# Kernel tuning notes

Hardware: AMD Instinct MI355X
Metric: run time of the kernel (lower is better)

The kernel has to match this reference:

```python
import jax, jax.numpy as jnp
import numpy as np

N_NODES = 50000
N_EDGES = 600000
D = 128
N_GRAPHS = 500


def setup_inputs() -> dict:
    key = jax.random.key(0)
    ks = jax.random.split(key, 8)
    node_feats = jax.random.normal(ks[0], (N_NODES, D), dtype=jnp.float32)
    W1 = jax.random.normal(ks[1], (D, D), dtype=jnp.float32) * (1.0 / np.sqrt(D))
    b1 = jnp.zeros((D,), dtype=jnp.float32)
    W2 = jax.random.normal(ks[2], (D, D), dtype=jnp.float32) * (1.0 / np.sqrt(D))
    b2 = jnp.zeros((D,), dtype=jnp.float32)
    src = jax.random.randint(ks[3], (N_EDGES,), 0, N_NODES, dtype=jnp.int32)
    dst = jax.random.randint(ks[4], (N_EDGES,), 0, N_NODES, dtype=jnp.int32)
    graph_ids = jnp.sort(jax.random.randint(ks[5], (N_NODES,), 0, N_GRAPHS, dtype=jnp.int32))
    return {"node_feats": node_feats, "W1": W1, "b1": b1, "W2": W2, "b2": b2,
            "src": src, "dst": dst, "graph_ids": graph_ids}


def _graph_conv(h, W, b, src, dst, norm_src, norm_dst, n_nodes):
    # DGL GraphConv, norm='both': D_in^{-1/2} A D_out^{-1/2} X W + b
    hs = h * norm_src[:, None]                     # (N, D) scale by out-degree^-1/2
    m = jax.ops.segment_sum(hs[src], dst, num_segments=n_nodes)  # sparse aggregate
    return (m * norm_dst[:, None]) @ W + b


def reference(node_feats, W1, b1, W2, b2, src, dst, graph_ids):
    n = node_feats.shape[0]
    ones_e = jnp.ones(src.shape, dtype=node_feats.dtype)
    deg_out = jnp.maximum(jax.ops.segment_sum(ones_e, src, num_segments=n), 1.0)
    deg_in = jnp.maximum(jax.ops.segment_sum(ones_e, dst, num_segments=n), 1.0)
    norm_src = deg_out ** -0.5
    norm_dst = deg_in ** -0.5
    # NOTE: original code builds num_layers-1 = 2 GraphConv layers for num_layers=3
    h = jax.nn.relu(_graph_conv(node_feats, W1, b1, src, dst, norm_src, norm_dst, n))
    h = jax.nn.relu(_graph_conv(h, W2, b2, src, dst, norm_src, norm_dst, n))
    # AvgPooling: per-graph mean of node features
    sums = jax.ops.segment_sum(h, graph_ids, num_segments=N_GRAPHS)
    counts = jnp.maximum(
        jax.ops.segment_sum(jnp.ones((n,), h.dtype), graph_ids, num_segments=N_GRAPHS), 1.0)
    return sums / counts[:, None]
```

## Files before the change

kernel.cpp:

```cpp
#include <hip/hip_runtime.h>

#define D 128

typedef __attribute__((ext_vector_type(8))) short bf16x8;
typedef __attribute__((ext_vector_type(4))) float f32x4;

__device__ __forceinline__ unsigned int f32_to_bf16_rne(float x) {
    unsigned int u = __float_as_uint(x);
    return (u + 0x7FFFu + ((u >> 16) & 1u)) >> 16;
}
__device__ __forceinline__ float bf16_val(float x) {
    return __uint_as_float(f32_to_bf16_rne(x) << 16);
}

__global__ void scatter_count_wprep_kernel(
    const int* __restrict__ src, const int* __restrict__ dst,
    int* __restrict__ cnt_out, int* __restrict__ deg_in,
    unsigned short* __restrict__ bucket, int E, int S, int eblocks,
    const float* __restrict__ W1, const float* __restrict__ W2,
    unsigned short* __restrict__ wt) {
    if ((int)blockIdx.x < eblocks) {
        int e = blockIdx.x * 256 + threadIdx.x;
        if (e < E) {
            int s = src[e];
            int d = dst[e];
            int pos = atomicAdd(&deg_in[d], 1);
            if (pos < S) bucket[(size_t)d * S + pos] = (unsigned short)s;
            atomicAdd(&cnt_out[s], 1);
        }
    } else {
        int i = (blockIdx.x - eblocks) * 256 + threadIdx.x;
        if (i < 2 * 16384) {
            int w = i >> 14, idx = i & 16383;
            int k = idx >> 7, col = idx & 127;
            float v = (w == 0 ? W1 : W2)[idx];
            unsigned int hi = f32_to_bf16_rne(v);
            float lo = v - __uint_as_float(hi << 16);
            int kc = k >> 5, quad = (k >> 3) & 3, j = k & 7;
            size_t slot = (size_t)kc * 4096 + quad * 1024 + col * 8 + j;
            wt[(size_t)w * 32768 + slot] = (unsigned short)hi;
            wt[(size_t)w * 32768 + 16384 + slot] = (unsigned short)f32_to_bf16_rne(lo);
        }
    }
}

__global__ void prep_kernel(const int* __restrict__ cnt_out, const int* __restrict__ cnt_in,
                            float* __restrict__ norm_src, float* __restrict__ norm_dst,
                            const float2* __restrict__ x, unsigned int* __restrict__ xb,
                            int N, int n2, int nbA) {
    int b = blockIdx.x;
    if (b < nbA) {
        int i = b * 256 + threadIdx.x;
        if (i < N) {
            norm_src[i] = 1.0f / sqrtf(fmaxf((float)cnt_out[i], 1.0f));
            norm_dst[i] = 1.0f / sqrtf(fmaxf((float)cnt_in[i], 1.0f));
        }
    } else {
        int i = (b - nbA) * 256 + threadIdx.x;
        if (i < n2) {
            int row = i >> 6;
            float s = 1.0f / sqrtf(fmaxf((float)cnt_out[row], 1.0f));
            float2 v = x[i];
            xb[i] = f32_to_bf16_rne(v.x * s) | (f32_to_bf16_rne(v.y * s) << 16);
        }
    }
}

#define AGG_STEP(J) do {                                                       \
        int sj = ss[J];                                                        \
        uint2 uj = featb2[(size_t)sj * 32 + c];                                \
        acc.x += __uint_as_float(uj.x << 16);                                  \
        acc.y += __uint_as_float(uj.x & 0xFFFF0000u);                          \
        acc.z += __uint_as_float(uj.y << 16);                                  \
        acc.w += __uint_as_float(uj.y & 0xFFFF0000u);                          \
    } while (0)

template <bool OUT_BF16>
__global__ __launch_bounds__(512, 8) void agg_mfma_kernel(
    const uint2* __restrict__ featb2, const float* __restrict__ norm_src,
    const float* __restrict__ norm_dst, const int* __restrict__ deg_in,
    const unsigned short* __restrict__ bucket,
    const unsigned short* __restrict__ wthi, const unsigned short* __restrict__ wtlo,
    const float* __restrict__ bias, void* __restrict__ outp, int N, int S) {
    __shared__ unsigned int mtp[2][16][68];
    int node0 = blockIdx.x * 16;
    int ng = threadIdx.x >> 5;
    int c  = threadIdx.x & 31;
    int node = node0 + ng;

    float4 acc = make_float4(0.f, 0.f, 0.f, 0.f);
    if (node < N) {
        int len = min(deg_in[node], S);
        const unsigned short* row = bucket + (size_t)node * S;
        int e = 0;
        for (; e + 8 <= len; e += 8) {
            ushort4 sa = *(const ushort4*)(row + e);
            ushort4 sb = *(const ushort4*)(row + e + 4);
            int ss[8] = {sa.x, sa.y, sa.z, sa.w, sb.x, sb.y, sb.z, sb.w};
            AGG_STEP(0); AGG_STEP(1); AGG_STEP(2); AGG_STEP(3);
            AGG_STEP(4); AGG_STEP(5); AGG_STEP(6); AGG_STEP(7);
        }
        for (; e + 4 <= len; e += 4) {
            ushort4 sa = *(const ushort4*)(row + e);
            int ss[4] = {sa.x, sa.y, sa.z, sa.w};
            AGG_STEP(0); AGG_STEP(1); AGG_STEP(2); AGG_STEP(3);
        }
        for (; e < len; e++) {
            int ss[1] = {row[e]};
            AGG_STEP(0);
        }
    }
    float hx = bf16_val(acc.x), hy = bf16_val(acc.y);
    float hz = bf16_val(acc.z), hw = bf16_val(acc.w);
    mtp[0][ng][2 * c]     = f32_to_bf16_rne(acc.x) | (f32_to_bf16_rne(acc.y) << 16);
    mtp[0][ng][2 * c + 1] = f32_to_bf16_rne(acc.z) | (f32_to_bf16_rne(acc.w) << 16);
    mtp[1][ng][2 * c]     = f32_to_bf16_rne(acc.x - hx) | (f32_to_bf16_rne(acc.y - hy) << 16);
    mtp[1][ng][2 * c + 1] = f32_to_bf16_rne(acc.z - hz) | (f32_to_bf16_rne(acc.w - hw) << 16);
    __syncthreads();

    int lane = threadIdx.x & 63;
    int wv   = threadIdx.x >> 6;
    int n16  = lane & 15;
    int quad = lane >> 4;
    int col  = wv * 16 + n16;
    f32x4 dacc = {0.f, 0.f, 0.f, 0.f};
#pragma unroll
    for (int kc = 0; kc < 4; kc++) {
        int ko = kc * 32 + quad * 8;
        int bo = kc * 4096 + quad * 1024 + col * 8;
        bf16x8 ahi = *(const bf16x8*)((const unsigned short*)mtp[0][n16] + ko);
        bf16x8 alo = *(const bf16x8*)((const unsigned short*)mtp[1][n16] + ko);
        bf16x8 bhi = *(const bf16x8*)(wthi + bo);
        bf16x8 blo = *(const bf16x8*)(wtlo + bo);
        dacc = __builtin_amdgcn_mfma_f32_16x16x32_bf16(ahi, bhi, dacc, 0, 0, 0);
        dacc = __builtin_amdgcn_mfma_f32_16x16x32_bf16(ahi, blo, dacc, 0, 0, 0);
        dacc = __builtin_amdgcn_mfma_f32_16x16x32_bf16(alo, bhi, dacc, 0, 0, 0);
    }
    float bv = bias[col];
#pragma unroll
    for (int r = 0; r < 4; r++) {
        int n = node0 + quad * 4 + r;
        if (n < N) {
            float v = fmaxf(fmaf(dacc[r], norm_dst[n], bv), 0.f);
            if (OUT_BF16) {
                ((unsigned short*)outp)[(size_t)n * D + col] =
                    (unsigned short)f32_to_bf16_rne(v * norm_src[n]);
            } else {
                ((float*)outp)[(size_t)n * D + col] = v;
            }
        }
    }
}

__global__ void pool_kernel(const float* __restrict__ h, const int* __restrict__ gids,
                            float* __restrict__ out, int N, int G) {
    __shared__ float part[128];
    int g = blockIdx.x;
    int f = threadIdx.x & 127;
    int half = threadIdx.x >> 7;
    int lo = 0, hi = N;
    while (lo < hi) { int mid = (lo + hi) >> 1; if (gids[mid] < g) lo = mid + 1; else hi = mid; }
    int start = lo;
    hi = N;
    while (lo < hi) { int mid = (lo + hi) >> 1; if (gids[mid] < g + 1) lo = mid + 1; else hi = mid; }
    int end = lo;

    float s0 = 0.f, s1 = 0.f, s2 = 0.f, s3 = 0.f;
    int n = start + half;
    for (; n + 6 < end; n += 8) {
        s0 += h[(size_t)(n + 0) * D + f];
        s1 += h[(size_t)(n + 2) * D + f];
        s2 += h[(size_t)(n + 4) * D + f];
        s3 += h[(size_t)(n + 6) * D + f];
    }
    for (; n < end; n += 2) s0 += h[(size_t)n * D + f];
    float s = (s0 + s1) + (s2 + s3);
    if (half == 1) part[f] = s;
    __syncthreads();
    if (half == 0) {
        float cnt = (float)(end - start);
        out[(size_t)g * D + f] = (s + part[f]) / fmaxf(cnt, 1.0f);
    }
}

extern "C" void kernel_launch(void* const* d_in, const int* in_sizes, int n_in,
                              void* d_out, int out_size, void* d_ws, size_t ws_size,
                              hipStream_t stream) {
    const float* node_feats = (const float*)d_in[0];
    const float* W1 = (const float*)d_in[1];
    const float* b1 = (const float*)d_in[2];
    const float* W2 = (const float*)d_in[3];
    const float* b2 = (const float*)d_in[4];
    const int*   src = (const int*)d_in[5];
    const int*   dst = (const int*)d_in[6];
    const int*   gid = (const int*)d_in[7];

    int N = in_sizes[7];
    int E = in_sizes[5];
    int G = out_size / D;

    size_t npad = ((size_t)N + 255) & ~(size_t)255;

    int S = 64;
    while (S > 32) {
        size_t need = (4 * npad + npad * (size_t)(S / 2)
                       + (size_t)N * D / 2 * 2
                       + (size_t)N * D
                       + 32768) * sizeof(float);
        if (need <= ws_size) break;
        S -= 16;
    }

    float* ws       = (float*)d_ws;
    float* norm_src = ws;
    float* norm_dst = ws + npad;
    int*   cnt_out  = (int*)(ws + 2 * npad);
    int*   deg_in   = (int*)(ws + 3 * npad);
    unsigned short* bucket = (unsigned short*)(ws + 4 * npad);
    unsigned int* xb  = (unsigned int*)(ws + 4 * npad + npad * (size_t)(S / 2));
    unsigned int* h1b = xb + (size_t)N * D / 2;
    float* h2       = (float*)(h1b + (size_t)N * D / 2);
    unsigned short* wt = (unsigned short*)(h2 + (size_t)N * D);
    float* out      = (float*)d_out;

    (void)hipMemsetAsync(cnt_out, 0, 2 * npad * sizeof(int), stream);
    int eblocks = (E + 255) / 256;
    int wblocks = (2 * 16384 + 255) / 256;
    scatter_count_wprep_kernel<<<eblocks + wblocks, 256, 0, stream>>>(
        src, dst, cnt_out, deg_in, bucket, E, S, eblocks, W1, W2, wt);
    int n2 = N * (D / 2);
    int nbA = (N + 255) / 256;
    int nbB = (n2 + 255) / 256;
    prep_kernel<<<nbA + nbB, 256, 0, stream>>>(cnt_out, deg_in, norm_src, norm_dst,
                                               (const float2*)node_feats, xb, N, n2, nbA);

    int blocks = (N + 15) / 16;

    agg_mfma_kernel<true><<<blocks, 512, 0, stream>>>(
        (const uint2*)xb, norm_src, norm_dst, deg_in, bucket,
        wt, wt + 16384, b1, h1b, N, S);
    agg_mfma_kernel<false><<<blocks, 512, 0, stream>>>(
        (const uint2*)h1b, norm_src, norm_dst, deg_in, bucket,
        wt + 32768, wt + 49152, b2, h2, N, S);

    pool_kernel<<<G, 256, 0, stream>>>(h2, gid, out, N, G);
}
```

Baseline: 223.2 us.

## Partition degree counting and bucketing per XCC to avoid cross-die atomics

The edge scatter now reads the hardware XCC id and does its degree and out-count atomics on per-XCC partitioned arrays, using workgroup-scope relaxed atomics, with per-XCC 16-slot buckets. A new merge kernel sums the eight partitions and compacts the per-XCC buckets into the final adjacency bucket. The aim is to keep atomics in each die's local L2 instead of paying for coherent device-wide atomics. In exchange it adds a kernel launch, a larger memset, and extra memory traffic. Workgroup-scope atomics are only correct if all blocks on an XCC share the same L2, and any XCC partition with more than 16 in-edges for a node now drops edges.

```diff
diff --git a/kernel.cpp b/kernel.cpp
--- a/kernel.cpp
+++ b/kernel.cpp
@@ -1,6 +1,7 @@
 #include <hip/hip_runtime.h>
 
 #define D 128
+#define S8 16
 
 typedef __attribute__((ext_vector_type(8))) short bf16x8;
 typedef __attribute__((ext_vector_type(4))) float f32x4;
@@ -15,18 +16,26 @@
 
 __global__ void scatter_count_wprep_kernel(
     const int* __restrict__ src, const int* __restrict__ dst,
-    int* __restrict__ cnt_out, int* __restrict__ deg_in,
-    unsigned short* __restrict__ bucket, int E, int S, int eblocks,
+    int* __restrict__ cnt_part,
+    int* __restrict__ deg_part,
+    unsigned short* __restrict__ bucket_part,
+    int E, int N, int npad, int eblocks,
     const float* __restrict__ W1, const float* __restrict__ W2,
     unsigned short* __restrict__ wt) {
     if ((int)blockIdx.x < eblocks) {
+        unsigned int xcc;
+        asm volatile("s_getreg_b32 %0, hwreg(HW_REG_XCC_ID)" : "=s"(xcc));
+        xcc &= 7u;
         int e = blockIdx.x * 256 + threadIdx.x;
         if (e < E) {
             int s = src[e];
             int d = dst[e];
-            int pos = atomicAdd(&deg_in[d], 1);
-            if (pos < S) bucket[(size_t)d * S + pos] = (unsigned short)s;
-            atomicAdd(&cnt_out[s], 1);
+            int pos = __hip_atomic_fetch_add(&deg_part[xcc * npad + d], 1,
+                                             __ATOMIC_RELAXED, __HIP_MEMORY_SCOPE_WORKGROUP);
+            if (pos < S8)
+                bucket_part[((size_t)xcc * N + d) * S8 + pos] = (unsigned short)s;
+            __hip_atomic_fetch_add(&cnt_part[xcc * npad + s], 1,
+                                   __ATOMIC_RELAXED, __HIP_MEMORY_SCOPE_WORKGROUP);
         }
     } else {
         int i = (blockIdx.x - eblocks) * 256 + threadIdx.x;
@@ -44,6 +53,33 @@
     }
 }
 
+__global__ void merge_compact_kernel(
+    const int* __restrict__ cnt_part, const int* __restrict__ deg_part,
+    const unsigned short* __restrict__ bucket_part,
+    int* __restrict__ cnt_out, int* __restrict__ deg_in,
+    unsigned short* __restrict__ bucket, int N, int npad, int S) {
+    int n = blockIdx.x * 256 + threadIdx.x;
+    if (n >= N) return;
+    int lens[8];
+    int totin = 0, totout = 0;
+#pragma unroll
+    for (int x = 0; x < 8; x++) {
+        lens[x] = deg_part[x * npad + n];
+        totin += lens[x];
+        totout += cnt_part[x * npad + n];
+    }
+    cnt_out[n] = totout;
+    deg_in[n]  = totin;
+    unsigned short* row = bucket + (size_t)n * S;
+    int off = 0;
+#pragma unroll
+    for (int x = 0; x < 8; x++) {
+        const unsigned short* pr = bucket_part + ((size_t)x * N + n) * S8;
+        int l = min(lens[x], S8);
+        for (int k = 0; k < l && off < S; k++) row[off++] = pr[k];
+    }
+}
+
 __global__ void prep_kernel(const int* __restrict__ cnt_out, const int* __restrict__ cnt_in,
                             float* __restrict__ norm_src, float* __restrict__ norm_dst,
                             const float2* __restrict__ x, unsigned int* __restrict__ xb,
@@ -223,11 +259,19 @@
     unsigned short* wt = (unsigned short*)(h2 + (size_t)N * D);
     float* out      = (float*)d_out;
 
-    (void)hipMemsetAsync(cnt_out, 0, 2 * npad * sizeof(int), stream);
+    int* deg_part = (int*)xb;
+    int* cnt_part = deg_part + 8 * (int)npad;
+    unsigned short* bucket_part = (unsigned short*)(cnt_part + 8 * (int)npad);
+
+    (void)hipMemsetAsync(deg_part, 0, 16 * npad * sizeof(int), stream);
     int eblocks = (E + 255) / 256;
     int wblocks = (2 * 16384 + 255) / 256;
     scatter_count_wprep_kernel<<<eblocks + wblocks, 256, 0, stream>>>(
-        src, dst, cnt_out, deg_in, bucket, E, S, eblocks, W1, W2, wt);
+        src, dst, cnt_part, deg_part, bucket_part, E, N, (int)npad, eblocks, W1, W2, wt);
+
+    merge_compact_kernel<<<((N + 255) / 256), 256, 0, stream>>>(
+        cnt_part, deg_part, bucket_part, cnt_out, deg_in, bucket, N, (int)npad, S);
+
     int n2 = N * (D / 2);
     int nbA = (N + 255) / 256;
     int nbB = (n2 + 255) / 256;
```

Result: slower. 234.3 us (+5.0%).

## Replace global atomic edge bucketing with per-block LDS histograms and scan

Applied to the files above, without the earlier changes.

Edge bucketing by destination no longer uses global atomics. Each of 128 blocks builds packed 8-bit per-node histograms of dst and src in shared memory and records a local rank per edge. A per-node scan over the blocks then produces offsets, in-degrees and norms, and a fill kernel scatters source ids into the buckets. This removes the global memset and the contended global atomics, but adds two extra launches, a scan pass that reads 128 histogram rows per node, and a limit of 255 per 8-bit counter. The resulting bucket order is deterministic, and the scratch data reuses the xb region before cvt overwrites it.

```diff
diff --git a/kernel.cpp b/kernel.cpp
--- a/kernel.cpp
+++ b/kernel.cpp
@@ -1,6 +1,8 @@
 #include <hip/hip_runtime.h>
 
 #define D 128
+#define NB 128
+#define NMAXW 12544
 
 typedef __attribute__((ext_vector_type(8))) short bf16x8;
 typedef __attribute__((ext_vector_type(4))) float f32x4;
@@ -13,23 +15,36 @@
     return __uint_as_float(f32_to_bf16_rne(x) << 16);
 }
 
-__global__ void scatter_count_wprep_kernel(
+__global__ __launch_bounds__(256) void hist_rank_wprep_kernel(
     const int* __restrict__ src, const int* __restrict__ dst,
-    int* __restrict__ cnt_out, int* __restrict__ deg_in,
-    unsigned short* __restrict__ bucket, int E, int S, int eblocks,
+    unsigned char* __restrict__ hist_dst,
+    unsigned char* __restrict__ hist_src,
+    unsigned char* __restrict__ rank8,
+    int E, int C, int W4, int eblocks,
     const float* __restrict__ W1, const float* __restrict__ W2,
     unsigned short* __restrict__ wt) {
-    if ((int)blockIdx.x < eblocks) {
-        int e = blockIdx.x * 256 + threadIdx.x;
-        if (e < E) {
-            int s = src[e];
-            int d = dst[e];
-            int pos = atomicAdd(&deg_in[d], 1);
-            if (pos < S) bucket[(size_t)d * S + pos] = (unsigned short)s;
-            atomicAdd(&cnt_out[s], 1);
-        }
+    __shared__ unsigned int histD[NMAXW];
+    __shared__ unsigned int histS[NMAXW];
+    int b = blockIdx.x;
+    if (b < eblocks) {
+        for (int w = threadIdx.x; w < W4; w += 256) { histD[w] = 0u; histS[w] = 0u; }
+        __syncthreads();
+        int e0 = b * C;
+        int e1 = min(e0 + C, E);
+        for (int e = e0 + threadIdx.x; e < e1; e += 256) {
+            int d_ = dst[e];
+            int s_ = src[e];
+            int sh = 8 * (d_ & 3);
+            unsigned int old = atomicAdd(&histD[d_ >> 2], 1u << sh);
+            atomicAdd(&histS[s_ >> 2], 1u << (8 * (s_ & 3)));
+            rank8[e] = (unsigned char)((old >> sh) & 255u);
+        }
+        __syncthreads();
+        unsigned int* rowD = (unsigned int*)(hist_dst + (size_t)b * (W4 * 4));
+        unsigned int* rowS = (unsigned int*)(hist_src + (size_t)b * (W4 * 4));
+        for (int w = threadIdx.x; w < W4; w += 256) { rowD[w] = histD[w]; rowS[w] = histS[w]; }
     } else {
-        int i = (blockIdx.x - eblocks) * 256 + threadIdx.x;
+        int i = (b - eblocks) * 256 + threadIdx.x;
         if (i < 2 * 16384) {
             int w = i >> 14, idx = i & 16383;
             int k = idx >> 7, col = idx & 127;
@@ -44,25 +59,52 @@
     }
 }
 
-__global__ void prep_kernel(const int* __restrict__ cnt_out, const int* __restrict__ cnt_in,
-                            float* __restrict__ norm_src, float* __restrict__ norm_dst,
-                            const float2* __restrict__ x, unsigned int* __restrict__ xb,
-                            int N, int n2, int nbA) {
+__global__ void scan_norms_kernel(
+    const unsigned char* __restrict__ hist_dst, const unsigned char* __restrict__ hist_src,
+    unsigned char* __restrict__ offs, int* __restrict__ deg_in,
+    float* __restrict__ norm_src, float* __restrict__ norm_dst, int N, int NR) {
+    int n = blockIdx.x * 256 + threadIdx.x;
+    if (n >= N) return;
+    int run = 0, cnt = 0;
+#pragma unroll 4
+    for (int b = 0; b < NB; b++) {
+        size_t idx = (size_t)b * NR + n;
+        offs[idx] = (unsigned char)min(run, 255);
+        run += hist_dst[idx];
+        cnt += hist_src[idx];
+    }
+    deg_in[n] = run;
+    norm_dst[n] = 1.0f / sqrtf(fmaxf((float)run, 1.0f));
+    norm_src[n] = 1.0f / sqrtf(fmaxf((float)cnt, 1.0f));
+}
+
+__global__ __launch_bounds__(256) void scatter_fill_kernel(
+    const int* __restrict__ src, const int* __restrict__ dst,
+    const unsigned char* __restrict__ rank8, const unsigned char* __restrict__ offs,
+    unsigned short* __restrict__ bucket, int E, int C, int W4, int S) {
+    __shared__ unsigned int offs_l[NMAXW];
     int b = blockIdx.x;
-    if (b < nbA) {
-        int i = b * 256 + threadIdx.x;
-        if (i < N) {
-            norm_src[i] = 1.0f / sqrtf(fmaxf((float)cnt_out[i], 1.0f));
-            norm_dst[i] = 1.0f / sqrtf(fmaxf((float)cnt_in[i], 1.0f));
-        }
-    } else {
-        int i = (b - nbA) * 256 + threadIdx.x;
-        if (i < n2) {
-            int row = i >> 6;
-            float s = 1.0f / sqrtf(fmaxf((float)cnt_out[row], 1.0f));
-            float2 v = x[i];
-            xb[i] = f32_to_bf16_rne(v.x * s) | (f32_to_bf16_rne(v.y * s) << 16);
-        }
+    const unsigned int* row = (const unsigned int*)(offs + (size_t)b * (W4 * 4));
+    for (int w = threadIdx.x; w < W4; w += 256) offs_l[w] = row[w];
+    __syncthreads();
+    int e0 = b * C;
+    int e1 = min(e0 + C, E);
+    for (int e = e0 + threadIdx.x; e < e1; e += 256) {
+        int d_ = dst[e];
+        int pos = (int)((offs_l[d_ >> 2] >> (8 * (d_ & 3))) & 255u) + (int)rank8[e];
+        if (pos < S) bucket[(size_t)d_ * S + pos] = (unsigned short)src[e];
+    }
+}
+
+__global__ void cvt_kernel(const float* __restrict__ norm_src,
+                           const float2* __restrict__ x, unsigned int* __restrict__ xb,
+                           int n2) {
+    int i = blockIdx.x * 256 + threadIdx.x;
+    if (i < n2) {
+        int row = i >> 6;
+        float s = norm_src[row];
+        float2 v = x[i];
+        xb[i] = f32_to_bf16_rne(v.x * s) | (f32_to_bf16_rne(v.y * s) << 16);
     }
 }
 
@@ -200,10 +242,13 @@
     int G = out_size / D;
 
     size_t npad = ((size_t)N + 255) & ~(size_t)255;
+    int W4 = (N + 3) / 4;
+    int NR = W4 * 4;
+    int C  = (E + NB - 1) / NB;
 
     int S = 64;
     while (S > 32) {
-        size_t need = (4 * npad + npad * (size_t)(S / 2)
+        size_t need = (3 * npad + npad * (size_t)(S / 2)
                        + (size_t)N * D / 2 * 2
                        + (size_t)N * D
                        + 32768) * sizeof(float);
@@ -214,25 +259,33 @@
     float* ws       = (float*)d_ws;
     float* norm_src = ws;
     float* norm_dst = ws + npad;
-    int*   cnt_out  = (int*)(ws + 2 * npad);
-    int*   deg_in   = (int*)(ws + 3 * npad);
-    unsigned short* bucket = (unsigned short*)(ws + 4 * npad);
-    unsigned int* xb  = (unsigned int*)(ws + 4 * npad + npad * (size_t)(S / 2));
+    int*   deg_in   = (int*)(ws + 2 * npad);
+    unsigned short* bucket = (unsigned short*)(ws + 3 * npad);
+    unsigned int* xb  = (unsigned int*)(ws + 3 * npad + npad * (size_t)(S / 2));
     unsigned int* h1b = xb + (size_t)N * D / 2;
     float* h2       = (float*)(h1b + (size_t)N * D / 2);
     unsigned short* wt = (unsigned short*)(h2 + (size_t)N * D);
     float* out      = (float*)d_out;
 
-    (void)hipMemsetAsync(cnt_out, 0, 2 * npad * sizeof(int), stream);
-    int eblocks = (E + 255) / 256;
+    unsigned char* tmp      = (unsigned char*)xb;
+    unsigned char* hist_dst = tmp;
+    unsigned char* hist_src = tmp + (size_t)NB * NR;
+    unsigned char* offs     = tmp + 2 * (size_t)NB * NR;
+    unsigned char* rank8    = tmp + 3 * (size_t)NB * NR;
+
     int wblocks = (2 * 16384 + 255) / 256;
-    scatter_count_wprep_kernel<<<eblocks + wblocks, 256, 0, stream>>>(
-        src, dst, cnt_out, deg_in, bucket, E, S, eblocks, W1, W2, wt);
+    hist_rank_wprep_kernel<<<NB + wblocks, 256, 0, stream>>>(
+        src, dst, hist_dst, hist_src, rank8, E, C, W4, NB, W1, W2, wt);
+
+    scan_norms_kernel<<<(N + 255) / 256, 256, 0, stream>>>(
+        hist_dst, hist_src, offs, deg_in, norm_src, norm_dst, N, NR);
+
+    scatter_fill_kernel<<<NB, 256, 0, stream>>>(
+        src, dst, rank8, offs, bucket, E, C, W4, S);
+
     int n2 = N * (D / 2);
-    int nbA = (N + 255) / 256;
-    int nbB = (n2 + 255) / 256;
-    prep_kernel<<<nbA + nbB, 256, 0, stream>>>(cnt_out, deg_in, norm_src, norm_dst,
-                                               (const float2*)node_feats, xb, N, n2, nbA);
+    cvt_kernel<<<(n2 + 255) / 256, 256, 0, stream>>>(
+        norm_src, (const float2*)node_feats, xb, n2);
 
     int blocks = (N + 15) / 16;
 
```

Result: faster. 212.5 us (-4.8%).
